# Kernel tuning notes

Hardware: AMD Instinct MI355X
Metric: run time of the kernel (lower is better)

## Reference

```python
import jax, jax.numpy as jnp
import numpy as np

T_DATA, E_NO, I_NO, SUB_NO = 10000, 2000, 500, 64
KERN_LEN, PAD = 201, 100


def setup_inputs() -> dict:
    key = jax.random.key(0)
    ks = jax.random.split(key, 8)
    S_e = (jax.random.uniform(ks[0], (T_DATA, E_NO)) < 0.05).astype(jnp.float32)
    S_i = (jax.random.uniform(ks[1], (T_DATA, I_NO)) < 0.05).astype(jnp.float32)
    # Synapse->subunit assignment: each synapse feeds exactly one subunit (one-hot rows of C_syn.T)
    ae = jax.random.randint(ks[2], (E_NO,), 0, SUB_NO)
    ai = jax.random.randint(ks[3], (I_NO,), 0, SUB_NO)
    C_syn_e = jax.nn.one_hot(ae, SUB_NO, dtype=jnp.float32).T  # [sub_no, E_no]
    C_syn_i = jax.nn.one_hot(ai, SUB_NO, dtype=jnp.float32).T  # [sub_no, I_no]
    # Sparse dendritic coupling matrix (binary tree-like connectivity)
    C_den = (jax.random.uniform(ks[4], (SUB_NO, SUB_NO)) < 0.05).astype(jnp.float32)
    # Learned raw parameters (per __init__: ones * init)
    weight_raw = jnp.zeros((SUB_NO, 2), jnp.float32)          # weight_init = 0.0
    decay_raw = jnp.full((SUB_NO,), 2.0, jnp.float32)         # decay_init = 2.0
    threshold_raw = jnp.zeros((SUB_NO,), jnp.float32)         # threshold_init = 0.0
    prop_raw = jnp.full((SUB_NO,), -1.0, jnp.float32)         # prop_init = -1.0
    return {"S_e": S_e, "S_i": S_i, "C_den": C_den, "C_syn_e": C_syn_e,
            "C_syn_i": C_syn_i, "weight_raw": weight_raw, "decay_raw": decay_raw,
            "threshold_raw": threshold_raw, "prop_raw": prop_raw}


def reference(S_e, S_i, C_den, C_syn_e, C_syn_i, weight_raw, decay_raw, threshold_raw, prop_raw):
    sub_no = C_den.shape[0]
    # Project presynaptic spikes onto subunits: [T, sub_no]
    syn_e = S_e @ C_syn_e.T
    syn_i = S_i @ C_syn_i.T
    weight_e = jnp.exp(weight_raw[:, 0])
    weight_i = -jnp.exp(weight_raw[:, 1])
    decay = jax.nn.sigmoid(decay_raw)
    threshold = -jnp.exp(threshold_raw)
    prop = jnpp = jnp.exp(prop_raw)
    drive = syn_e * weight_e[None, :] + syn_i * weight_i[None, :]  # [T, sub_no]

    def step_fn(carry, d_t):
        V, spk = carry
        # reset-on-spike, leak, synaptic drive, dendritic propagation of spikes
        V = V * (1.0 - spk) * decay + d_t + (spk * prop) @ C_den.T
        spk = jnp.heaviside(V + threshold, jnp.float32(0.0))
        return (V, spk), spk

    init = (jnp.zeros(sub_no, jnp.float32), jnp.zeros(sub_no, jnp.float32))
    _, spk_out = jax.lax.scan(step_fn, init, drive)  # spk_out: [T, sub_no]

    # Alpha-kernel smoothing of root subunit spike train (Tau, W are fixed buffers)
    t_tau = jnp.arange(KERN_LEN, dtype=jnp.float32) / jnp.exp(jnp.float32(2.0))
    kern = t_tau * jnp.exp(-t_tau) * jnp.exp(jnp.float32(0.75))
    kern_flipped = jnp.flip(kern)
    x = spk_out[:, 0][None, None, :]               # [1,1,T]
    w = kern_flipped[None, None, :]                # [1,1,201]
    final = jax.lax.conv_general_dilated(x, w, (1,), [(PAD, PAD)]).reshape(-1)
    return final, spk_out
```

## Files before the change

kernel.cpp:

```cpp
#include <hip/hip_runtime.h>
#include <math.h>

#define T_DATA 10000
#define E_NO 2000
#define I_NO 500
#define SUB_NO 64
#define KERN_LEN 201
#define PAD 100
#define NBLK 314


__global__ void assign_kernel(const float* __restrict__ Ce, const float* __restrict__ Ci,
                              int* __restrict__ ae, int* __restrict__ ai) {
    int idx = blockIdx.x * 256 + threadIdx.x;
    if (idx < E_NO) {
        int a = 0;
        for (int s = 0; s < SUB_NO; ++s)
            if (Ce[(size_t)s * E_NO + idx] != 0.0f) a = s;
        ae[idx] = a;
    } else if (idx < E_NO + I_NO) {
        int i = idx - E_NO;
        int a = 0;
        for (int s = 0; s < SUB_NO; ++s)
            if (Ci[(size_t)s * I_NO + i] != 0.0f) a = s;
        ai[i] = a;
    }
}

__global__ void drive_kernel(const float* __restrict__ Se, const float* __restrict__ Si,
                             const float* __restrict__ wraw,
                             const int* __restrict__ ae, const int* __restrict__ ai,
                             float* __restrict__ drive) {
    __shared__ float be[SUB_NO];
    __shared__ float bi[SUB_NO];
    int t = blockIdx.x;
    int tid = threadIdx.x;
    if (tid < SUB_NO) { be[tid] = 0.0f; bi[tid] = 0.0f; }
    __syncthreads();
    const float* se = Se + (size_t)t * E_NO;
    for (int e = tid; e < E_NO; e += 256) {
        if (se[e] != 0.0f) atomicAdd(&be[ae[e]], 1.0f);
    }
    const float* si = Si + (size_t)t * I_NO;
    for (int i = tid; i < I_NO; i += 256) {
        if (si[i] != 0.0f) atomicAdd(&bi[ai[i]], 1.0f);
    }
    __syncthreads();
    if (tid < SUB_NO) {
        float we = (float)exp((double)wraw[2 * tid]);
        float wi = -(float)exp((double)wraw[2 * tid + 1]);
        drive[(size_t)t * SUB_NO + tid] =
            __fadd_rn(__fmul_rn(be[tid], we), __fmul_rn(bi[tid], wi));
    }
}

template<int KBITS>
__device__ __forceinline__ void scan_fast(const float* drive, unsigned int* packed,
                                          unsigned long long rowmask, float p0,
                                          float decay, float thr, int s) {
    constexpr int NT = 1 << KBITS;
    float tbl[NT];
    {
        float f = 0.0f;
#pragma unroll
        for (int i = 0; i < NT; ++i) { tbl[i] = f; f = __fadd_rn(f, p0); }
    }

    float V = 0.0f;
    bool sp = false;
    unsigned long long mask = 0ull;
    unsigned int bits = 0u;

    const float* dp = drive + s;
    unsigned int* pw = packed + s;

    float bufA[32], bufB[32];
#pragma unroll
    for (int k = 0; k < 32; ++k) bufA[k] = dp[(size_t)k * SUB_NO];

    auto STEP = [&](float d, unsigned int bit) {
        unsigned long long m = mask & rowmask;
        int kc = (int)__popcll(m);
        float v[NT / 2];
#pragma unroll
        for (int i = 0; i < NT / 2; ++i) v[i] = (kc & 1) ? tbl[2 * i + 1] : tbl[2 * i];
#pragma unroll
        for (int lvl = 1; lvl < KBITS; ++lvl) {
            const int n = NT >> (lvl + 1);
#pragma unroll
            for (int i = 0; i < n; ++i)
                v[i] = (kc & (1 << lvl)) ? v[2 * i + 1] : v[2 * i];
        }
        float acc = v[0];
        float Vr = sp ? 0.0f : V;
        float bb = __fmul_rn(Vr, decay);
        float cc = __fadd_rn(bb, d);
        V = __fadd_rn(cc, acc);
        float sv = __fadd_rn(V, thr);
        sp = sv > 0.0f;
        mask = __ballot(sp);
        bits |= sp ? bit : 0u;
    };

    for (int b = 0; b < NBLK; b += 2) {
#pragma unroll
        for (int k = 0; k < 32; ++k)
            bufB[k] = dp[((size_t)(b + 1) * 32 + k) * SUB_NO];
        bits = 0u;
#pragma unroll
        for (int k = 0; k < 32; ++k) STEP(bufA[k], 1u << k);
        pw[(size_t)b * SUB_NO] = bits;

#pragma unroll
        for (int k = 0; k < 32; ++k)
            bufA[k] = dp[((size_t)(b + 2) * 32 + k) * SUB_NO];
        bits = 0u;
#pragma unroll
        for (int k = 0; k < 32; ++k) STEP(bufB[k], 1u << k);
        pw[(size_t)(b + 1) * SUB_NO] = bits;
    }
}

__device__ void scan_slow(const float* drive, unsigned int* packed,
                          unsigned long long rowmask, const float* prop_l,
                          float decay, float thr, int s) {
    float V = 0.0f;
    bool sp = false;
    unsigned long long mask = 0ull;
    for (int b = 0; b < NBLK; ++b) {
        unsigned int bits = 0u;
        for (int k = 0; k < 32; ++k) {
            int t = b * 32 + k;
            float d = drive[(size_t)t * SUB_NO + s];
            unsigned long long m = mask & rowmask;
            float acc = 0.0f;
            for (int j = 0; j < SUB_NO; ++j) {
                float c = ((m >> j) & 1ull) ? prop_l[j] : 0.0f;
                acc = __fadd_rn(acc, c);
            }
            float Vr = sp ? 0.0f : V;
            float bb = __fmul_rn(Vr, decay);
            float cc = __fadd_rn(bb, d);
            V = __fadd_rn(cc, acc);
            float sv = __fadd_rn(V, thr);
            sp = sv > 0.0f;
            mask = __ballot(sp);
            bits |= sp ? (1u << k) : 0u;
        }
        packed[(size_t)b * SUB_NO + s] = bits;
    }
}

__global__ void __launch_bounds__(64, 1)
scan_kernel(const float* drive, const float* __restrict__ Cden,
            const float* __restrict__ decay_raw, const float* __restrict__ thr_raw,
            const float* __restrict__ prop_raw, unsigned int* packed) {
    __shared__ float prop_l[SUB_NO];
    int s = threadIdx.x;
    prop_l[s] = (float)exp((double)prop_raw[s]);
    __syncthreads();
    float myp = prop_l[s];

    float em = (float)exp(-(double)decay_raw[s]);
    float den = __fadd_rn(1.0f, em);
    float decay = (float)(1.0 / (double)den);
    float thr = -(float)exp((double)thr_raw[s]);

    unsigned long long rowmask = 0ull;
    for (int j = 0; j < SUB_NO; ++j)
        if (Cden[(size_t)s * SUB_NO + j] != 0.0f) rowmask |= (1ull << j);

    float p0 = prop_l[0];
    bool uni = __all(myp == p0);
    int maxk = (int)__popcll(rowmask);
    for (int off = 32; off; off >>= 1) {
        int o = __shfl_xor(maxk, off);
        maxk = maxk > o ? maxk : o;
    }

    if (uni && maxk <= 7)       scan_fast<3>(drive, packed, rowmask, p0, decay, thr, s);
    else if (uni && maxk <= 15) scan_fast<4>(drive, packed, rowmask, p0, decay, thr, s);
    else                        scan_slow(drive, packed, rowmask, prop_l, decay, thr, s);
}

__global__ void expand_kernel(const unsigned int* __restrict__ packed,
                              float* __restrict__ spk_out) {
    int idx = blockIdx.x * 256 + threadIdx.x;
    int t = idx >> 6, s = idx & 63;
    unsigned int w = packed[(size_t)(t >> 5) * SUB_NO + s];
    spk_out[idx] = (float)((w >> (t & 31)) & 1u);
}

__global__ void conv_kernel(const unsigned int* __restrict__ packed,
                            float* __restrict__ out) {
    __shared__ float kern_s[KERN_LEN];
    __shared__ float x_s[256 + 2 * PAD];
    int tid = threadIdx.x;
    int t0 = blockIdx.x * 256;

    float e2 = (float)exp(2.0);
    float e075 = (float)exp(0.75);
    for (int m = tid; m < KERN_LEN; m += 256) {
        float tt = (float)m / e2;
        kern_s[m] = __fmul_rn(__fmul_rn(tt, expf(-tt)), e075);
    }
    for (int k = tid; k < 256 + 2 * PAD; k += 256) {
        int idx = t0 - PAD + k;
        float xv = 0.0f;
        if (idx >= 0 && idx < T_DATA) {
            unsigned int w = packed[(size_t)(idx >> 5) * SUB_NO];
            xv = (float)((w >> (idx & 31)) & 1u);
        }
        x_s[k] = xv;
    }
    __syncthreads();

    int t = t0 + tid;
    if (t < T_DATA) {
        float acc = 0.0f;
        for (int m = 0; m < KERN_LEN; ++m)
            acc += kern_s[m] * x_s[tid + 2 * PAD - m];
        out[t] = acc;
    }
}

extern "C" void kernel_launch(void* const* d_in, const int* in_sizes, int n_in,
                              void* d_out, int out_size, void* d_ws, size_t ws_size,
                              hipStream_t stream) {
    const float* S_e      = (const float*)d_in[0];
    const float* S_i      = (const float*)d_in[1];
    const float* C_den    = (const float*)d_in[2];
    const float* C_syn_e  = (const float*)d_in[3];
    const float* C_syn_i  = (const float*)d_in[4];
    const float* w_raw    = (const float*)d_in[5];
    const float* dec_raw  = (const float*)d_in[6];
    const float* thr_raw  = (const float*)d_in[7];
    const float* prop_raw = (const float*)d_in[8];

    float* out = (float*)d_out;
    float* ws = (float*)d_ws;
    float* drive = ws;
    int*   ae    = (int*)(ws + 640000);
    int*   ai    = (int*)(ws + 642000);

    size_t need_bytes = (size_t)(642500 + NBLK * SUB_NO) * 4;
    unsigned int* packed = (ws_size >= need_bytes)
                               ? (unsigned int*)(ws + 642500)
                               : (unsigned int*)ws;

    assign_kernel<<<(E_NO + I_NO + 255) / 256, 256, 0, stream>>>(C_syn_e, C_syn_i, ae, ai);
    drive_kernel<<<T_DATA, 256, 0, stream>>>(S_e, S_i, w_raw, ae, ai, drive);
    scan_kernel<<<1, 64, 0, stream>>>(drive, C_den, dec_raw, thr_raw, prop_raw, packed);
    expand_kernel<<<T_DATA * SUB_NO / 256, 256, 0, stream>>>(packed, out + T_DATA);
    conv_kernel<<<(T_DATA + 255) / 256, 256, 0, stream>>>(packed, out);
}
```

Measured before the change: 610.4 us.

## Replace lookup-tree prop sum with multiply when exact; use scalar-mask selects

Adds a linear scan path that computes the propagated input as popcount times prop, in place of the table-and-select tree. It is taken only after a runtime check that sequential float addition of prop equals k*prop for every relevant k. The tree and linear paths now use inline v_cndmask with wave ballot masks for the reset and bit packing, compare V against the positive threshold directly, and add a 5-bit tree variant. The drive kernel reads spike rows as float4. The serial scan's per-step dependency chain becomes shorter, at the cost of inline asm and a small bit-exactness check at kernel start.

New measurement: 552.2 us. 9.5% less time.

```diff
diff --git a/kernel.cpp b/kernel.cpp
--- a/kernel.cpp
+++ b/kernel.cpp
@@ -9,6 +9,17 @@
 #define PAD 100
 #define NBLK 314
 
+__device__ __forceinline__ float sel_f(float a0, float b1, unsigned long long m) {
+    float r;
+    asm("v_cndmask_b32 %0, %1, %2, %3" : "=v"(r) : "v"(a0), "v"(b1), "s"(m));
+    return r;
+}
+__device__ __forceinline__ unsigned int sel_u(unsigned int a0, unsigned int b1,
+                                              unsigned long long m) {
+    unsigned int r;
+    asm("v_cndmask_b32 %0, %1, %2, %3" : "=v"(r) : "v"(a0), "v"(b1), "s"(m));
+    return r;
+}
 
 __global__ void assign_kernel(const float* __restrict__ Ce, const float* __restrict__ Ci,
                               int* __restrict__ ae, int* __restrict__ ai) {
@@ -37,13 +48,23 @@
     int tid = threadIdx.x;
     if (tid < SUB_NO) { be[tid] = 0.0f; bi[tid] = 0.0f; }
     __syncthreads();
-    const float* se = Se + (size_t)t * E_NO;
-    for (int e = tid; e < E_NO; e += 256) {
-        if (se[e] != 0.0f) atomicAdd(&be[ae[e]], 1.0f);
-    }
-    const float* si = Si + (size_t)t * I_NO;
-    for (int i = tid; i < I_NO; i += 256) {
-        if (si[i] != 0.0f) atomicAdd(&bi[ai[i]], 1.0f);
+    const float4* se4 = (const float4*)(Se + (size_t)t * E_NO);
+    for (int e4 = tid; e4 < E_NO / 4; e4 += 256) {
+        float4 v = se4[e4];
+        int b = e4 * 4;
+        if (v.x != 0.0f) atomicAdd(&be[ae[b + 0]], 1.0f);
+        if (v.y != 0.0f) atomicAdd(&be[ae[b + 1]], 1.0f);
+        if (v.z != 0.0f) atomicAdd(&be[ae[b + 2]], 1.0f);
+        if (v.w != 0.0f) atomicAdd(&be[ae[b + 3]], 1.0f);
+    }
+    const float4* si4 = (const float4*)(Si + (size_t)t * I_NO);
+    for (int i4 = tid; i4 < I_NO / 4; i4 += 256) {
+        float4 v = si4[i4];
+        int b = i4 * 4;
+        if (v.x != 0.0f) atomicAdd(&bi[ai[b + 0]], 1.0f);
+        if (v.y != 0.0f) atomicAdd(&bi[ai[b + 1]], 1.0f);
+        if (v.z != 0.0f) atomicAdd(&bi[ai[b + 2]], 1.0f);
+        if (v.w != 0.0f) atomicAdd(&bi[ai[b + 3]], 1.0f);
     }
     __syncthreads();
     if (tid < SUB_NO) {
@@ -54,10 +75,54 @@
     }
 }
 
+__device__ void scan_lin(const float* __restrict__ drive, unsigned int* __restrict__ packed,
+                         unsigned long long rowmask, float p0,
+                         float decay, float thrpos, int s) {
+    float V = 0.0f;
+    unsigned long long mask = 0ull;
+    const float* dp = drive + s;
+    unsigned int* pw = packed + s;
+    unsigned int row_lo = (unsigned int)rowmask;
+    unsigned int row_hi = (unsigned int)(rowmask >> 32);
+    float zerof = 0.0f;
+    unsigned int bits = 0u;
+
+    float bufA[32], bufB[32];
+#pragma unroll
+    for (int k = 0; k < 32; ++k) bufA[k] = dp[(size_t)k * SUB_NO];
+
+    auto STEP = [&](float d, unsigned int bitk) {
+        unsigned int kc = __popc(((unsigned int)mask) & row_lo)
+                        + __popc(((unsigned int)(mask >> 32)) & row_hi);
+        float acc = __fmul_rn((float)kc, p0);
+        float Vr = sel_f(V, zerof, mask);
+        float bb = __fmul_rn(Vr, decay);
+        float cc = __fadd_rn(bb, d);
+        V = __fadd_rn(cc, acc);
+        mask = __ballot(V > thrpos);
+        bits = sel_u(bits, bits | bitk, mask);
+    };
+
+    for (int b = 0; b < NBLK; b += 2) {
+#pragma unroll
+        for (int k = 0; k < 32; ++k) bufB[k] = dp[((size_t)(b + 1) * 32 + k) * SUB_NO];
+        bits = 0u;
+#pragma unroll
+        for (int k = 0; k < 32; ++k) STEP(bufA[k], 1u << k);
+        pw[(size_t)b * SUB_NO] = bits;
+#pragma unroll
+        for (int k = 0; k < 32; ++k) bufA[k] = dp[((size_t)(b + 2) * 32 + k) * SUB_NO];
+        bits = 0u;
+#pragma unroll
+        for (int k = 0; k < 32; ++k) STEP(bufB[k], 1u << k);
+        pw[(size_t)(b + 1) * SUB_NO] = bits;
+    }
+}
+
 template<int KBITS>
-__device__ __forceinline__ void scan_fast(const float* drive, unsigned int* packed,
-                                          unsigned long long rowmask, float p0,
-                                          float decay, float thr, int s) {
+__device__ void scan_tree(const float* __restrict__ drive, unsigned int* __restrict__ packed,
+                          unsigned long long rowmask, float p0,
+                          float decay, float thrpos, int s) {
     constexpr int NT = 1 << KBITS;
     float tbl[NT];
     {
@@ -65,55 +130,52 @@
 #pragma unroll
         for (int i = 0; i < NT; ++i) { tbl[i] = f; f = __fadd_rn(f, p0); }
     }
-
     float V = 0.0f;
-    bool sp = false;
     unsigned long long mask = 0ull;
-    unsigned int bits = 0u;
-
     const float* dp = drive + s;
     unsigned int* pw = packed + s;
+    unsigned int row_lo = (unsigned int)rowmask;
+    unsigned int row_hi = (unsigned int)(rowmask >> 32);
+    float zerof = 0.0f;
+    unsigned int bits = 0u;
 
     float bufA[32], bufB[32];
 #pragma unroll
     for (int k = 0; k < 32; ++k) bufA[k] = dp[(size_t)k * SUB_NO];
 
-    auto STEP = [&](float d, unsigned int bit) {
-        unsigned long long m = mask & rowmask;
-        int kc = (int)__popcll(m);
+    auto STEP = [&](float d, unsigned int bitk) {
+        unsigned int kc = __popc(((unsigned int)mask) & row_lo)
+                        + __popc(((unsigned int)(mask >> 32)) & row_hi);
+        unsigned long long lm[KBITS];
+#pragma unroll
+        for (int l = 0; l < KBITS; ++l) lm[l] = __ballot(kc & (1u << l));
         float v[NT / 2];
 #pragma unroll
-        for (int i = 0; i < NT / 2; ++i) v[i] = (kc & 1) ? tbl[2 * i + 1] : tbl[2 * i];
-#pragma unroll
-        for (int lvl = 1; lvl < KBITS; ++lvl) {
-            const int n = NT >> (lvl + 1);
-#pragma unroll
-            for (int i = 0; i < n; ++i)
-                v[i] = (kc & (1 << lvl)) ? v[2 * i + 1] : v[2 * i];
+        for (int i = 0; i < NT / 2; ++i) v[i] = sel_f(tbl[2 * i], tbl[2 * i + 1], lm[0]);
+#pragma unroll
+        for (int l = 1; l < KBITS; ++l) {
+            const int n = NT >> (l + 1);
+#pragma unroll
+            for (int i = 0; i < n; ++i) v[i] = sel_f(v[2 * i], v[2 * i + 1], lm[l]);
         }
         float acc = v[0];
-        float Vr = sp ? 0.0f : V;
+        float Vr = sel_f(V, zerof, mask);
         float bb = __fmul_rn(Vr, decay);
         float cc = __fadd_rn(bb, d);
         V = __fadd_rn(cc, acc);
-        float sv = __fadd_rn(V, thr);
-        sp = sv > 0.0f;
-        mask = __ballot(sp);
-        bits |= sp ? bit : 0u;
+        mask = __ballot(V > thrpos);
+        bits = sel_u(bits, bits | bitk, mask);
     };
 
     for (int b = 0; b < NBLK; b += 2) {
 #pragma unroll
-        for (int k = 0; k < 32; ++k)
-            bufB[k] = dp[((size_t)(b + 1) * 32 + k) * SUB_NO];
+        for (int k = 0; k < 32; ++k) bufB[k] = dp[((size_t)(b + 1) * 32 + k) * SUB_NO];
         bits = 0u;
 #pragma unroll
         for (int k = 0; k < 32; ++k) STEP(bufA[k], 1u << k);
         pw[(size_t)b * SUB_NO] = bits;
-
-#pragma unroll
-        for (int k = 0; k < 32; ++k)
-            bufA[k] = dp[((size_t)(b + 2) * 32 + k) * SUB_NO];
+#pragma unroll
+        for (int k = 0; k < 32; ++k) bufA[k] = dp[((size_t)(b + 2) * 32 + k) * SUB_NO];
         bits = 0u;
 #pragma unroll
         for (int k = 0; k < 32; ++k) STEP(bufB[k], 1u << k);
@@ -164,7 +226,8 @@
     float em = (float)exp(-(double)decay_raw[s]);
     float den = __fadd_rn(1.0f, em);
     float decay = (float)(1.0 / (double)den);
-    float thr = -(float)exp((double)thr_raw[s]);
+    float thrpos = (float)exp((double)thr_raw[s]);
+    float thr = -thrpos;
 
     unsigned long long rowmask = 0ull;
     for (int j = 0; j < SUB_NO; ++j)
@@ -178,8 +241,15 @@
         maxk = maxk > o ? maxk : o;
     }
 
-    if (uni && maxk <= 7)       scan_fast<3>(drive, packed, rowmask, p0, decay, thr, s);
-    else if (uni && maxk <= 15) scan_fast<4>(drive, packed, rowmask, p0, decay, thr, s);
+    float seqk = 0.0f;
+    for (int i = 0; i < s; ++i) seqk = __fadd_rn(seqk, p0);
+    bool lok = (s > maxk) || (seqk == __fmul_rn((float)s, p0));
+    bool uselin = uni && __all(lok);
+
+    if (uselin)                 scan_lin(drive, packed, rowmask, p0, decay, thrpos, s);
+    else if (uni && maxk <= 7)  scan_tree<3>(drive, packed, rowmask, p0, decay, thrpos, s);
+    else if (uni && maxk <= 15) scan_tree<4>(drive, packed, rowmask, p0, decay, thrpos, s);
+    else if (uni && maxk <= 31) scan_tree<5>(drive, packed, rowmask, p0, decay, thrpos, s);
     else                        scan_slow(drive, packed, rowmask, prop_l, decay, thr, s);
 }
 
```

## Rewrite serial spike scan in inline GCN assembly with multiply-based propagation sum

Applied to the files above, without the earlier changes.

Replaces the templated select-tree scan with hand-written inline assembly that computes the dendritic propagation sum as popcount times prop, used when repeated addition equals that product. Otherwise it falls back to a ds_bpermute table lookup. The step is reordered so the next leak-plus-drive term is precomputed off the critical dependency chain. The drive kernel also moves to float4 loads. The serial 10000-step recurrence latency is the target, and it relies on exact float equivalence checks and fragile register-heavy asm.

Measured after the change: 554.0 us. 1.1x faster.

```diff
diff --git a/kernel.cpp b/kernel.cpp
--- a/kernel.cpp
+++ b/kernel.cpp
@@ -8,7 +8,6 @@
 #define KERN_LEN 201
 #define PAD 100
 #define NBLK 314
-
 
 __global__ void assign_kernel(const float* __restrict__ Ce, const float* __restrict__ Ci,
                               int* __restrict__ ae, int* __restrict__ ai) {
@@ -37,13 +36,23 @@
     int tid = threadIdx.x;
     if (tid < SUB_NO) { be[tid] = 0.0f; bi[tid] = 0.0f; }
     __syncthreads();
-    const float* se = Se + (size_t)t * E_NO;
-    for (int e = tid; e < E_NO; e += 256) {
-        if (se[e] != 0.0f) atomicAdd(&be[ae[e]], 1.0f);
-    }
-    const float* si = Si + (size_t)t * I_NO;
-    for (int i = tid; i < I_NO; i += 256) {
-        if (si[i] != 0.0f) atomicAdd(&bi[ai[i]], 1.0f);
+    const float4* se4 = (const float4*)(Se + (size_t)t * E_NO);
+    for (int e4 = tid; e4 < E_NO / 4; e4 += 256) {
+        float4 v = se4[e4];
+        int b = e4 * 4;
+        if (v.x != 0.0f) atomicAdd(&be[ae[b + 0]], 1.0f);
+        if (v.y != 0.0f) atomicAdd(&be[ae[b + 1]], 1.0f);
+        if (v.z != 0.0f) atomicAdd(&be[ae[b + 2]], 1.0f);
+        if (v.w != 0.0f) atomicAdd(&be[ae[b + 3]], 1.0f);
+    }
+    const float4* si4 = (const float4*)(Si + (size_t)t * I_NO);
+    for (int i4 = tid; i4 < I_NO / 4; i4 += 256) {
+        float4 v = si4[i4];
+        int b = i4 * 4;
+        if (v.x != 0.0f) atomicAdd(&bi[ai[b + 0]], 1.0f);
+        if (v.y != 0.0f) atomicAdd(&bi[ai[b + 1]], 1.0f);
+        if (v.z != 0.0f) atomicAdd(&bi[ai[b + 2]], 1.0f);
+        if (v.w != 0.0f) atomicAdd(&bi[ai[b + 3]], 1.0f);
     }
     __syncthreads();
     if (tid < SUB_NO) {
@@ -54,70 +63,116 @@
     }
 }
 
-template<int KBITS>
-__device__ __forceinline__ void scan_fast(const float* drive, unsigned int* packed,
-                                          unsigned long long rowmask, float p0,
-                                          float decay, float thr, int s) {
-    constexpr int NT = 1 << KBITS;
-    float tbl[NT];
-    {
-        float f = 0.0f;
-#pragma unroll
-        for (int i = 0; i < NT; ++i) { tbl[i] = f; f = __fadd_rn(f, p0); }
-    }
-
-    float V = 0.0f;
-    bool sp = false;
-    unsigned long long mask = 0ull;
-    unsigned int bits = 0u;
-
+#define S_LIN(DK, DK1, LIT) \
+  "v_and_b32 %[tlo], vcc_lo, %[rlo]\n\t" \
+  "v_and_b32 %[thi], vcc_hi, %[rhi]\n\t" \
+  "v_cndmask_b32 %[base], %[w0], %[" DK "], vcc\n\t" \
+  "v_bcnt_u32_b32 %[kc], %[tlo], 0\n\t" \
+  "v_bcnt_u32_b32 %[kc], %[thi], %[kc]\n\t" \
+  "v_cvt_f32_u32 %[kf], %[kc]\n\t" \
+  "v_mul_f32 %[acc], %[kf], %[pp]\n\t" \
+  "v_add_f32 %[vv], %[base], %[acc]\n\t" \
+  "v_cmp_gt_f32 vcc, %[vv], %[thr]\n\t" \
+  "v_mul_f32 %[w0], %[vv], %[dec]\n\t" \
+  "v_add_f32 %[w0], %[w0], %[" DK1 "]\n\t" \
+  "v_or_b32 %[tmp], " LIT ", %[bits]\n\t" \
+  "v_cndmask_b32 %[bits], %[bits], %[tmp], vcc\n\t"
+
+#define S_BP(DK, DK1, LIT) \
+  "v_and_b32 %[tlo], vcc_lo, %[rlo]\n\t" \
+  "v_and_b32 %[thi], vcc_hi, %[rhi]\n\t" \
+  "v_cndmask_b32 %[base], %[w0], %[" DK "], vcc\n\t" \
+  "v_bcnt_u32_b32 %[kc], %[tlo], 0\n\t" \
+  "v_bcnt_u32_b32 %[kc], %[thi], %[kc]\n\t" \
+  "v_lshlrev_b32 %[kc], 2, %[kc]\n\t" \
+  "ds_bpermute_b32 %[acc], %[kc], %[vtab]\n\t" \
+  "s_waitcnt lgkmcnt(0)\n\t" \
+  "v_add_f32 %[vv], %[base], %[acc]\n\t" \
+  "v_cmp_gt_f32 vcc, %[vv], %[thr]\n\t" \
+  "v_mul_f32 %[w0], %[vv], %[dec]\n\t" \
+  "v_add_f32 %[w0], %[w0], %[" DK1 "]\n\t" \
+  "v_or_b32 %[tmp], " LIT ", %[bits]\n\t" \
+  "v_cndmask_b32 %[bits], %[bits], %[tmp], vcc\n\t"
+
+#define STEPS32(S) \
+  S("d0","d1","1")            S("d1","d2","2")            S("d2","d3","4")            S("d3","d4","8") \
+  S("d4","d5","16")           S("d5","d6","32")           S("d6","d7","64")           S("d7","d8","0x80") \
+  S("d8","d9","0x100")        S("d9","d10","0x200")       S("d10","d11","0x400")      S("d11","d12","0x800") \
+  S("d12","d13","0x1000")     S("d13","d14","0x2000")     S("d14","d15","0x4000")     S("d15","d16","0x8000") \
+  S("d16","d17","0x10000")    S("d17","d18","0x20000")    S("d18","d19","0x40000")    S("d19","d20","0x80000") \
+  S("d20","d21","0x100000")   S("d21","d22","0x200000")   S("d22","d23","0x400000")   S("d23","d24","0x800000") \
+  S("d24","d25","0x1000000")  S("d25","d26","0x2000000")  S("d26","d27","0x4000000")  S("d27","d28","0x8000000") \
+  S("d28","d29","0x10000000") S("d29","d30","0x20000000") S("d30","d31","0x40000000") S("d31","d32","0x80000000")
+
+#define RUN_BLOCK(STEPSTR, B) do { \
+    unsigned int _tlo, _thi, _kc, _tmp, _bits; float _kf, _acc, _base; \
+    unsigned long long _mout; \
+    asm volatile( \
+        "s_mov_b64 vcc, %[min]\n\t" \
+        "v_mov_b32 %[bits], 0\n\t" \
+        "s_nop 1\n\t" \
+        STEPSTR \
+        "s_mov_b64 %[mout], vcc\n\t" \
+        : [vv]"+v"(V), [w0]"+v"(w0), [bits]"=&v"(_bits), [mout]"=s"(_mout), \
+          [tlo]"=&v"(_tlo), [thi]"=&v"(_thi), [kc]"=&v"(_kc), [tmp]"=&v"(_tmp), \
+          [kf]"=&v"(_kf), [acc]"=&v"(_acc), [base]"=&v"(_base) \
+        : [min]"s"(m), [rlo]"v"(row_lo), [rhi]"v"(row_hi), [pp]"v"(p0), \
+          [dec]"v"(decay), [thr]"v"(thrpos), [vtab]"v"(vtab), \
+          [d0]"v"(B[0]),  [d1]"v"(B[1]),  [d2]"v"(B[2]),  [d3]"v"(B[3]), \
+          [d4]"v"(B[4]),  [d5]"v"(B[5]),  [d6]"v"(B[6]),  [d7]"v"(B[7]), \
+          [d8]"v"(B[8]),  [d9]"v"(B[9]),  [d10]"v"(B[10]), [d11]"v"(B[11]), \
+          [d12]"v"(B[12]), [d13]"v"(B[13]), [d14]"v"(B[14]), [d15]"v"(B[15]), \
+          [d16]"v"(B[16]), [d17]"v"(B[17]), [d18]"v"(B[18]), [d19]"v"(B[19]), \
+          [d20]"v"(B[20]), [d21]"v"(B[21]), [d22]"v"(B[22]), [d23]"v"(B[23]), \
+          [d24]"v"(B[24]), [d25]"v"(B[25]), [d26]"v"(B[26]), [d27]"v"(B[27]), \
+          [d28]"v"(B[28]), [d29]"v"(B[29]), [d30]"v"(B[30]), [d31]"v"(B[31]), \
+          [d32]"v"(B[32]) \
+        : "vcc"); \
+    m = _mout; bitsv = _bits; } while (0)
+
+__device__ void scan_lin_asm(const float* drive, unsigned int* packed,
+                             unsigned int row_lo, unsigned int row_hi, float p0,
+                             float decay, float thrpos, float vtab, int s) {
     const float* dp = drive + s;
     unsigned int* pw = packed + s;
-
-    float bufA[32], bufB[32];
-#pragma unroll
-    for (int k = 0; k < 32; ++k) bufA[k] = dp[(size_t)k * SUB_NO];
-
-    auto STEP = [&](float d, unsigned int bit) {
-        unsigned long long m = mask & rowmask;
-        int kc = (int)__popcll(m);
-        float v[NT / 2];
-#pragma unroll
-        for (int i = 0; i < NT / 2; ++i) v[i] = (kc & 1) ? tbl[2 * i + 1] : tbl[2 * i];
-#pragma unroll
-        for (int lvl = 1; lvl < KBITS; ++lvl) {
-            const int n = NT >> (lvl + 1);
-#pragma unroll
-            for (int i = 0; i < n; ++i)
-                v[i] = (kc & (1 << lvl)) ? v[2 * i + 1] : v[2 * i];
-        }
-        float acc = v[0];
-        float Vr = sp ? 0.0f : V;
-        float bb = __fmul_rn(Vr, decay);
-        float cc = __fadd_rn(bb, d);
-        V = __fadd_rn(cc, acc);
-        float sv = __fadd_rn(V, thr);
-        sp = sv > 0.0f;
-        mask = __ballot(sp);
-        bits |= sp ? bit : 0u;
-    };
-
+    float bufA[33], bufB[33];
+#pragma unroll
+    for (int k = 0; k < 33; ++k) bufA[k] = dp[(size_t)k * SUB_NO];
+    float V = 0.0f, w0 = bufA[0];
+    unsigned long long m = 0ull;
+    unsigned int bitsv;
     for (int b = 0; b < NBLK; b += 2) {
 #pragma unroll
-        for (int k = 0; k < 32; ++k)
-            bufB[k] = dp[((size_t)(b + 1) * 32 + k) * SUB_NO];
-        bits = 0u;
-#pragma unroll
-        for (int k = 0; k < 32; ++k) STEP(bufA[k], 1u << k);
-        pw[(size_t)b * SUB_NO] = bits;
-
-#pragma unroll
-        for (int k = 0; k < 32; ++k)
-            bufA[k] = dp[((size_t)(b + 2) * 32 + k) * SUB_NO];
-        bits = 0u;
-#pragma unroll
-        for (int k = 0; k < 32; ++k) STEP(bufB[k], 1u << k);
-        pw[(size_t)(b + 1) * SUB_NO] = bits;
+        for (int k = 0; k < 33; ++k) bufB[k] = dp[((size_t)(b + 1) * 32 + k) * SUB_NO];
+        RUN_BLOCK(STEPS32(S_LIN), bufA);
+        pw[(size_t)b * SUB_NO] = bitsv;
+#pragma unroll
+        for (int k = 0; k < 33; ++k) bufA[k] = dp[((size_t)(b + 2) * 32 + k) * SUB_NO];
+        RUN_BLOCK(STEPS32(S_LIN), bufB);
+        pw[(size_t)(b + 1) * SUB_NO] = bitsv;
+    }
+}
+
+__device__ void scan_bp_asm(const float* drive, unsigned int* packed,
+                            unsigned int row_lo, unsigned int row_hi, float p0,
+                            float decay, float thrpos, float vtab, int s) {
+    const float* dp = drive + s;
+    unsigned int* pw = packed + s;
+    float bufA[33], bufB[33];
+#pragma unroll
+    for (int k = 0; k < 33; ++k) bufA[k] = dp[(size_t)k * SUB_NO];
+    float V = 0.0f, w0 = bufA[0];
+    unsigned long long m = 0ull;
+    unsigned int bitsv;
+    for (int b = 0; b < NBLK; b += 2) {
+#pragma unroll
+        for (int k = 0; k < 33; ++k) bufB[k] = dp[((size_t)(b + 1) * 32 + k) * SUB_NO];
+        RUN_BLOCK(STEPS32(S_BP), bufA);
+        pw[(size_t)b * SUB_NO] = bitsv;
+#pragma unroll
+        for (int k = 0; k < 33; ++k) bufA[k] = dp[((size_t)(b + 2) * 32 + k) * SUB_NO];
+        RUN_BLOCK(STEPS32(S_BP), bufB);
+        pw[(size_t)(b + 1) * SUB_NO] = bitsv;
     }
 }
 
@@ -132,10 +187,10 @@
         for (int k = 0; k < 32; ++k) {
             int t = b * 32 + k;
             float d = drive[(size_t)t * SUB_NO + s];
-            unsigned long long m = mask & rowmask;
+            unsigned long long mm = mask & rowmask;
             float acc = 0.0f;
             for (int j = 0; j < SUB_NO; ++j) {
-                float c = ((m >> j) & 1ull) ? prop_l[j] : 0.0f;
+                float c = ((mm >> j) & 1ull) ? prop_l[j] : 0.0f;
                 acc = __fadd_rn(acc, c);
             }
             float Vr = sp ? 0.0f : V;
@@ -164,11 +219,14 @@
     float em = (float)exp(-(double)decay_raw[s]);
     float den = __fadd_rn(1.0f, em);
     float decay = (float)(1.0 / (double)den);
-    float thr = -(float)exp((double)thr_raw[s]);
+    float thrpos = (float)exp((double)thr_raw[s]);
+    float thr = -thrpos;
 
     unsigned long long rowmask = 0ull;
     for (int j = 0; j < SUB_NO; ++j)
         if (Cden[(size_t)s * SUB_NO + j] != 0.0f) rowmask |= (1ull << j);
+    unsigned int row_lo = (unsigned int)rowmask;
+    unsigned int row_hi = (unsigned int)(rowmask >> 32);
 
     float p0 = prop_l[0];
     bool uni = __all(myp == p0);
@@ -178,9 +236,19 @@
         maxk = maxk > o ? maxk : o;
     }
 
-    if (uni && maxk <= 7)       scan_fast<3>(drive, packed, rowmask, p0, decay, thr, s);
-    else if (uni && maxk <= 15) scan_fast<4>(drive, packed, rowmask, p0, decay, thr, s);
-    else                        scan_slow(drive, packed, rowmask, prop_l, decay, thr, s);
+    float seqk = 0.0f;
+    for (int i = 0; i < s; ++i) seqk = __fadd_rn(seqk, p0);
+    float vtab = seqk;
+
+    bool lok = (s > maxk) || (seqk == __fmul_rn((float)s, p0));
+    bool uselin = uni && __all(lok);
+
+    if (uselin)
+        scan_lin_asm(drive, packed, row_lo, row_hi, p0, decay, thrpos, vtab, s);
+    else if (uni)
+        scan_bp_asm(drive, packed, row_lo, row_hi, p0, decay, thrpos, vtab, s);
+    else
+        scan_slow(drive, packed, rowmask, prop_l, decay, thr, s);
 }
 
 __global__ void expand_kernel(const unsigned int* __restrict__ packed,
```
